# Kernel tuning notes

Hardware: AMD Instinct MI355X
Metric: run time of the kernel (lower is better)

Reference implementation:

```python
import jax, jax.numpy as jnp
import numpy as np

D_MODEL = 1024
NUM_HEADS = 16
THETA = 10000.0


def _rope(x, cos, sin):
    # x: [B, H, S, dk]; cos/sin: [B, 1, S, dk//2]
    x1 = x[..., 0::2]
    x2 = x[..., 1::2]
    r1 = x1 * cos - x2 * sin
    r2 = x1 * sin + x2 * cos
    return jnp.stack([r1, r2], axis=-1).reshape(x.shape)


def setup_inputs() -> dict:
    key = jax.random.key(0)
    ks = jax.random.split(key, 5)
    B, S, D = 2, 2048, D_MODEL
    std = np.sqrt(2.0 / (D + D))
    x = jax.random.normal(ks[0], (B, S, D), dtype=jnp.float32)
    Wq = jax.random.normal(ks[1], (D, D), dtype=jnp.float32) * std
    Wk = jax.random.normal(ks[2], (D, D), dtype=jnp.float32) * std
    Wv = jax.random.normal(ks[3], (D, D), dtype=jnp.float32) * std
    Wo = jax.random.normal(ks[4], (D, D), dtype=jnp.float32) * std
    token_positions = jnp.broadcast_to(jnp.arange(S, dtype=jnp.int32), (B, S))
    return {"x": x, "Wq": Wq, "Wk": Wk, "Wv": Wv, "Wo": Wo,
            "token_positions": token_positions}


def reference(x, Wq, Wk, Wv, Wo, token_positions):
    B, S, D = x.shape
    H = NUM_HEADS
    dk = D // H

    def split_heads(t):  # [B,S,D] -> [B,H,S,dk]
        return t.reshape(B, S, H, dk).transpose(0, 2, 1, 3)

    Q = split_heads(x @ Wq)
    K = split_heads(x @ Wk)
    V = split_heads(x @ Wv)

    # RoPE angles: theta^(-2i/dk) frequencies, indexed by token positions
    freqs = THETA ** (-jnp.arange(0, dk, 2, dtype=jnp.float32) / dk)  # [dk/2]
    angles = token_positions.astype(jnp.float32)[..., None] * freqs   # [B,S,dk/2]
    cos = jnp.cos(angles)[:, None]  # [B,1,S,dk/2] broadcast over heads
    sin = jnp.sin(angles)[:, None]
    Q = _rope(Q, cos, sin)
    K = _rope(K, cos, sin)

    scores = jnp.einsum('bhqd,bhkd->bhqk', Q, K) / jnp.sqrt(jnp.float32(dk))
    causal = jnp.tril(jnp.ones((S, S), dtype=bool))  # [S,S]
    scores = jnp.where(causal[None, None], scores, -jnp.inf)
    probs = jax.nn.softmax(scores, axis=-1)
    att = jnp.einsum('bhqk,bhkd->bhqd', probs, V)  # [B,H,S,dk]
    att = att.transpose(0, 2, 1, 3).reshape(B, S, D)
    return att @ Wo
```

## Files before the change

kernel.cpp:

```cpp
#include <hip/hip_runtime.h>
#include <math.h>

#define SLEN 2048
#define DMODEL 1024
#define NHEADS 16
#define DK 64
#define NBATCH 2
#define M_TOT (NBATCH * SLEN)
#define NQKV (3 * DMODEL)

typedef __bf16 bf16x8 __attribute__((ext_vector_type(8)));
typedef float f32x4 __attribute__((ext_vector_type(4)));
typedef float f32x16 __attribute__((ext_vector_type(16)));

static __device__ __forceinline__ unsigned short f2bf(float f) {
    unsigned int u = __float_as_uint(f);
    u += 0x7fffu + ((u >> 16) & 1u);
    return (unsigned short)(u >> 16);
}

static __device__ __forceinline__ unsigned cvtpk(float a, float b) {
    unsigned r;
    asm("v_cvt_pk_bf16_f32 %0, %1, %2" : "=v"(r) : "v"(a), "v"(b));
    return r;
}

#if __has_builtin(__builtin_amdgcn_exp2f)
#define EXP2(x) __builtin_amdgcn_exp2f(x)
#else
#define EXP2(x) exp2f(x)
#endif

static __device__ __forceinline__ void gload16(const void* g, void* l) {
    __builtin_amdgcn_global_load_lds(
        (const __attribute__((address_space(1))) unsigned int*)g,
        (__attribute__((address_space(3))) unsigned int*)l, 16, 0, 0);
}

__global__ __launch_bounds__(256)
void prep_all(const float* __restrict__ x,
              const float* __restrict__ Wq, const float* __restrict__ Wk,
              const float* __restrict__ Wv, const float* __restrict__ Wo,
              unsigned short* __restrict__ xb,
              unsigned short* __restrict__ Wcat,
              unsigned short* __restrict__ Wot)
{
    __shared__ float t[64][65];
    const int blk = blockIdx.x;
    const int tid = threadIdx.x;
    if (blk < 4096) {
        int i = blk * 256 + tid;
        float4 v = *(const float4*)&x[(size_t)i * 4];
        ushort4 o;
        o.x = f2bf(v.x); o.y = f2bf(v.y); o.z = f2bf(v.z); o.w = f2bf(v.w);
        *(ushort4*)&xb[(size_t)i * 4] = o;
    } else {
        const int tt = blk - 4096;
        const int widx = tt >> 8;
        const int t256 = tt & 255;
        const float* W = (widx == 0) ? Wq : (widx == 1) ? Wk : (widx == 2) ? Wv : Wo;
        unsigned short* Wt = (widx < 3) ? (Wcat + (size_t)widx * 1048576) : Wot;
        const int c0 = (t256 & 15) * 64, r0 = (t256 >> 4) * 64;
        const int tr = tid >> 4, tc = (tid & 15) * 4;
        #pragma unroll
        for (int rr = 0; rr < 4; ++rr) {
            int row = rr * 16 + tr;
            float4 v = *(const float4*)&W[(size_t)(r0 + row) * DMODEL + c0 + tc];
            t[row][tc + 0] = v.x; t[row][tc + 1] = v.y;
            t[row][tc + 2] = v.z; t[row][tc + 3] = v.w;
        }
        __syncthreads();
        #pragma unroll
        for (int rr = 0; rr < 4; ++rr) {
            int orow = rr * 16 + tr;
            ushort4 o;
            o.x = f2bf(t[tc + 0][orow]);
            o.y = f2bf(t[tc + 1][orow]);
            o.z = f2bf(t[tc + 2][orow]);
            o.w = f2bf(t[tc + 3][orow]);
            *(ushort4*)&Wt[(size_t)(c0 + orow) * DMODEL + r0 + tc] = o;
        }
    }
}

template<int BM, int BN, int MODE>
__global__ __launch_bounds__(256)
void gemm_mfma(const unsigned short* __restrict__ A,
               const unsigned short* __restrict__ Bt,
               float* __restrict__ C,
               unsigned short* __restrict__ Qd,
               unsigned short* __restrict__ Kd,
               unsigned short* __restrict__ Vtd,
               const int* __restrict__ pos,
               int N, int K)
{
    constexpr int MR = BM / 32;
    constexpr int NR = BN / 32;
    __shared__ unsigned short AB[(BM + BN) * 64];
    const int tid = threadIdx.x;
    const int w = tid >> 6, l = tid & 63;
    const int m0 = blockIdx.y * BM, n0 = blockIdx.x * BN;
    const int wr = (w >> 1) * (BM / 2), wc = (w & 1) * (BN / 2);
    const int lr = l >> 3, lp = l & 7;

    f32x4 acc[MR][NR] = {};

    unsigned short* As = AB;
    unsigned short* Bs = AB + BM * 64;

    for (int k0 = 0; k0 < K; k0 += 64) {
        #pragma unroll
        for (int i = 0; i < BM / 32; ++i) {
            int row = i * 32 + w * 8 + lr;
            int s = lp ^ (row & 7);
            gload16(A + (size_t)(m0 + row) * K + k0 + s * 8, (void*)(As + (i * 32 + w * 8) * 64));
        }
        #pragma unroll
        for (int i = 0; i < BN / 32; ++i) {
            int row = i * 32 + w * 8 + lr;
            int s = lp ^ (row & 7);
            gload16(Bt + (size_t)(n0 + row) * K + k0 + s * 8, (void*)(Bs + (i * 32 + w * 8) * 64));
        }
        __syncthreads();
        #pragma unroll
        for (int ks = 0; ks < 2; ++ks) {
            bf16x8 af[MR], bfr[NR];
            #pragma unroll
            for (int i = 0; i < MR; ++i) {
                int row = wr + i * 16 + (l & 15);
                int slot = (ks * 4 + (l >> 4)) ^ (row & 7);
                af[i] = *(const bf16x8*)((const char*)As + row * 128 + slot * 16);
            }
            #pragma unroll
            for (int j = 0; j < NR; ++j) {
                int row = wc + j * 16 + (l & 15);
                int slot = (ks * 4 + (l >> 4)) ^ (row & 7);
                bfr[j] = *(const bf16x8*)((const char*)Bs + row * 128 + slot * 16);
            }
            __builtin_amdgcn_s_setprio(1);
            #pragma unroll
            for (int i = 0; i < MR; ++i)
                #pragma unroll
                for (int j = 0; j < NR; ++j)
                    acc[i][j] = __builtin_amdgcn_mfma_f32_16x16x32_bf16(af[i], bfr[j], acc[i][j], 0, 0, 0);
            __builtin_amdgcn_s_setprio(0);
        }
        __syncthreads();
    }

    if (MODE == 0) {
        #pragma unroll
        for (int i = 0; i < MR; ++i)
            #pragma unroll
            for (int j = 0; j < NR; ++j)
                #pragma unroll
                for (int r = 0; r < 4; ++r) {
                    int row = m0 + wr + i * 16 + (l >> 4) * 4 + r;
                    int col = n0 + wc + j * 16 + (l & 15);
                    C[(size_t)row * N + col] = acc[i][j][r];
                }
    } else {
        const int seg = (n0 + wc) >> 10;
        #pragma unroll
        for (int i = 0; i < MR; ++i) {
            const int mbase = m0 + wr + i * 16 + (l >> 4) * 4;
            #pragma unroll
            for (int j = 0; j < NR; ++j) {
                const int n = n0 + wc + j * 16 + (l & 15);
                const int h = (n >> 6) & 15;
                const int d = n & 63;
                if (seg < 2) {
                    unsigned short* dst = (seg == 0) ? Qd : Kd;
                    const int de = d & ~1;
                    const float freq = __expf((float)de * (-9.210340371976184f / 64.f));
                    #pragma unroll
                    for (int r = 0; r < 4; ++r) {
                        const int m = mbase + r;
                        const int b = m >> 11, s = m & 2047;
                        float v = acc[i][j][r];
                        float p2 = __shfl_xor(v, 1);
                        float ang = (float)pos[m] * freq;
                        float sn, cs;
                        __sincosf(ang, &sn, &cs);
                        float res = ((l & 1) == 0) ? (v * cs - p2 * sn) : (p2 * sn + v * cs);
                        if (seg == 0) res *= 0.18033688011112042f;
                        dst[((size_t)(b * NHEADS + h) * SLEN + s) * DK + d] = f2bf(res);
                    }
                } else {
                    const int b = mbase >> 11, s0 = mbase & 2047;
                    const int tile = s0 >> 5, ksv = (s0 >> 4) & 1, hb = (s0 >> 3) & 1, j0 = s0 & 7;
                    const int mt2v = d >> 5, c31v = d & 31;
                    size_t idx = (size_t)(b * NHEADS + h) * 131072 + tile * 2048
                               + ksv * 1024 + mt2v * 512 + hb * 256 + c31v * 8 + j0;
                    ushort4 o;
                    o.x = f2bf(acc[i][j][0]); o.y = f2bf(acc[i][j][1]);
                    o.z = f2bf(acc[i][j][2]); o.w = f2bf(acc[i][j][3]);
                    *(ushort4*)&Vtd[idx] = o;
                }
            }
        }
    }
}

__global__ __launch_bounds__(128)
void attn_mfma(const unsigned short* __restrict__ Q,
               const unsigned short* __restrict__ K,
               const unsigned short* __restrict__ Vf,
               unsigned short* __restrict__ Oa)
{
    __shared__ char smem[17408];
    const int tid = threadIdx.x;
    const int w = tid >> 6, l = tid & 63;
    const int h = l >> 5, c31 = l & 31;

    const int id = blockIdx.x;
    const int bh = (id & 7) * 4 + ((id >> 3) & 3);
    const int g  = 63 - (id >> 5);
    const int n_w = (g >= w) ? ((g - w) >> 1) + 1 : 0;

    const unsigned short* Qb  = Q  + (size_t)bh * SLEN * DK;
    const unsigned short* Kb  = K  + (size_t)bh * SLEN * DK;
    const unsigned short* VfB = Vf + (size_t)bh * 131072;

    const int q_g = g * 32 + c31;

    bf16x8 qf[4];
    #pragma unroll
    for (int kb = 0; kb < 4; ++kb)
        qf[kb] = *(const bf16x8*)(Qb + (size_t)q_g * DK + kb * 16 + h * 8);

    float lsum = 0.f;
    f32x16 oacc[2] = {};

    char* mybuf = smem + w * 8192;
    auto STAGE = [&](int t, int p) {
        char* dst = mybuf + p * 4096;
        const unsigned short* src = Kb + (size_t)t * 2048;
        #pragma unroll
        for (int i2 = 0; i2 < 4; ++i2) {
            int row = i2 * 8 + (l >> 3);
            gload16(src + row * 64 + (((l & 7) ^ (row & 7)) * 8), dst + i2 * 1024);
        }
    };

    if (n_w > 0) {
        STAGE(w, 0);
        if (n_w > 1) STAGE(w + 2, 1);

        for (int i = 0; i < n_w; ++i) {
            const int t = w + 2 * i;
            const bool last = (i == n_w - 1);
            if (last) { asm volatile("s_waitcnt vmcnt(0)" ::: "memory"); }
            else      { asm volatile("s_waitcnt vmcnt(4)" ::: "memory"); }
            __builtin_amdgcn_sched_barrier(0);

            bf16x8 vf0, vf1, vf2, vf3;
            {
                const unsigned short* vsrc = VfB + (size_t)t * 2048 + l * 8;
                vf0 = *(const bf16x8*)(vsrc);
                vf1 = *(const bf16x8*)(vsrc + 512);
                vf2 = *(const bf16x8*)(vsrc + 1024);
                vf3 = *(const bf16x8*)(vsrc + 1536);
            }

            const char* kbuf = mybuf + (i & 1) * 4096;
            f32x16 sacc = {};
            __builtin_amdgcn_s_setprio(1);
            #pragma unroll
            for (int kb = 0; kb < 4; ++kb) {
                bf16x8 kf = *(const bf16x8*)(kbuf + c31 * 128 + ((((kb * 2 + h)) ^ (c31 & 7)) << 4));
                sacc = __builtin_amdgcn_mfma_f32_32x32x16_bf16(kf, qf[kb], sacc, 0, 0, 0);
            }
            __builtin_amdgcn_s_setprio(0);

            if (last && w == (g & 1)) {
                #pragma unroll
                for (int r = 0; r < 16; ++r) {
                    int crow = (r & 3) + 8 * (r >> 2) + 4 * h;
                    if (crow > c31) sacc[r] = -1e30f;
                }
            }

            float ps = 0.f;
            #pragma unroll
            for (int r = 0; r < 16; ++r) {
                float e = EXP2(sacc[r]);
                sacc[r] = e;
                ps += e;
            }
            lsum += ps;

            #pragma unroll
            for (int ks = 0; ks < 2; ++ks) {
                const int rb = ks * 8;
                unsigned pk0 = cvtpk(sacc[rb + 0], sacc[rb + 1]);
                unsigned pk1 = cvtpk(sacc[rb + 2], sacc[rb + 3]);
                unsigned pk2 = cvtpk(sacc[rb + 4], sacc[rb + 5]);
                unsigned pk3 = cvtpk(sacc[rb + 6], sacc[rb + 7]);
                asm("v_permlane32_swap_b32 %0, %1" : "+v"(pk0), "+v"(pk2));
                asm("v_permlane32_swap_b32 %0, %1" : "+v"(pk1), "+v"(pk3));
                union { unsigned u[4]; bf16x8 v; } pf;
                pf.u[0] = pk0;
                pf.u[1] = pk1;
                pf.u[2] = pk2;
                pf.u[3] = pk3;
                __builtin_amdgcn_s_setprio(1);
                oacc[0] = __builtin_amdgcn_mfma_f32_32x32x16_bf16(ks ? vf2 : vf0, pf.v, oacc[0], 0, 0, 0);
                oacc[1] = __builtin_amdgcn_mfma_f32_32x32x16_bf16(ks ? vf3 : vf1, pf.v, oacc[1], 0, 0, 0);
                __builtin_amdgcn_s_setprio(0);
            }

            if (i + 2 < n_w) STAGE(w + 2 * (i + 2), i & 1);
        }
    }

    __syncthreads();
    float* Ll = (float*)(smem + 16384);
    Ll[(w * 2 + h) * 32 + c31] = lsum;
    __syncthreads();
    const float lstar = Ll[c31] + Ll[32 + c31] + Ll[64 + c31] + Ll[96 + c31];

    float* Op = (float*)smem;
    if (w == 0) {
        #pragma unroll
        for (int mt = 0; mt < 2; ++mt)
            #pragma unroll
            for (int r = 0; r < 16; ++r)
                Op[(mt * 16 + r) * 64 + l] = oacc[mt][r];
    }
    __syncthreads();
    if (w == 1) {
        const float inv = 1.f / lstar;
        unsigned short* Os = (unsigned short*)(smem + 8192);
        #pragma unroll
        for (int mt = 0; mt < 2; ++mt)
            #pragma unroll
            for (int rq = 0; rq < 4; ++rq) {
                float a0 = (Op[(mt * 16 + rq * 4 + 0) * 64 + l] + oacc[mt][rq * 4 + 0]) * inv;
                float a1 = (Op[(mt * 16 + rq * 4 + 1) * 64 + l] + oacc[mt][rq * 4 + 1]) * inv;
                float a2 = (Op[(mt * 16 + rq * 4 + 2) * 64 + l] + oacc[mt][rq * 4 + 2]) * inv;
                float a3 = (Op[(mt * 16 + rq * 4 + 3) * 64 + l] + oacc[mt][rq * 4 + 3]) * inv;
                uint2 pv;
                pv.x = cvtpk(a0, a1);
                pv.y = cvtpk(a2, a3);
                int dbyte = mt * 64 + rq * 16 + h * 8;
                *(uint2*)((char*)Os + c31 * 128 + (dbyte ^ ((c31 & 7) << 4))) = pv;
            }
        const int b = bh >> 4, hh = bh & 15;
        const int cc = l & 7;
        #pragma unroll
        for (int pp = 0; pp < 4; ++pp) {
            int row = pp * 8 + (l >> 3);
            uint4 vv = *(const uint4*)((const char*)Os + row * 128 + ((cc ^ (row & 7)) << 4));
            int srow = g * 32 + row;
            *(uint4*)&Oa[((size_t)(b * SLEN + srow)) * DMODEL + hh * DK + cc * 8] = vv;
        }
    }
}

extern "C" void kernel_launch(void* const* d_in, const int* in_sizes, int n_in,
                              void* d_out, int out_size, void* d_ws, size_t ws_size,
                              hipStream_t stream)
{
    const float* x  = (const float*)d_in[0];
    const float* Wq = (const float*)d_in[1];
    const float* Wk = (const float*)d_in[2];
    const float* Wv = (const float*)d_in[3];
    const float* Wo = (const float*)d_in[4];
    const int*  pos = (const int*)d_in[5];
    float* out = (float*)d_out;

    char* ws = (char*)d_ws;
    const size_t MB = 1024 * 1024;
    unsigned short* xb   = (unsigned short*)(ws);
    unsigned short* Wcat = (unsigned short*)(ws + 8 * MB);
    unsigned short* Wot  = (unsigned short*)(ws + 14 * MB);
    unsigned short* Qws  = (unsigned short*)(ws + 16 * MB);
    unsigned short* Kws  = (unsigned short*)(ws + 24 * MB);
    unsigned short* Vfws = (unsigned short*)(ws + 32 * MB);
    unsigned short* attb = (unsigned short*)(ws + 40 * MB);

    prep_all<<<5120, 256, 0, stream>>>(x, Wq, Wk, Wv, Wo, xb, Wcat, Wot);

    gemm_mfma<128, 128, 1><<<dim3(NQKV / 128, M_TOT / 128), 256, 0, stream>>>(
        xb, Wcat, nullptr, Qws, Kws, Vfws, pos, NQKV, DMODEL);

    attn_mfma<<<2048, 128, 0, stream>>>(Qws, Kws, Vfws, attb);

    gemm_mfma<64, 128, 0><<<dim3(DMODEL / 128, M_TOT / 64), 256, 0, stream>>>(
        attb, Wot, out, nullptr, nullptr, nullptr, nullptr, DMODEL, DMODEL);
}
```

Measured before the change: 100.00 us.

## Pre-pack weights in MFMA fragment order and load B directly to registers

The weight transpose/convert prep kernel now writes bf16 weights in a layout that matches the 16x16x32 MFMA B-operand fragment order. The GEMM then loads B fragments straight from global memory into registers, with no LDS staging, and its shared buffer holds only A. This removes LDS traffic and bank pressure for B and halves the GEMM's shared-memory footprint. In exchange, each wave now fetches B from global or L2 with no reuse across the waves of a block, and it adds register pressure.

Result: slower. 104.3 us (+4.3%).

```diff
diff --git a/kernel.cpp b/kernel.cpp
--- a/kernel.cpp
+++ b/kernel.cpp
@@ -70,15 +70,20 @@
             t[row][tc + 2] = v.z; t[row][tc + 3] = v.w;
         }
         __syncthreads();
+        const int t2 = (r0 >> 5) + (tc >> 5);
+        const int q  = (tc >> 3) & 3;
+        const int e  = tc & 7;
         #pragma unroll
         for (int rr = 0; rr < 4; ++rr) {
             int orow = rr * 16 + tr;
+            const int n = c0 + orow;
+            const int G = n >> 4, n15 = n & 15;
             ushort4 o;
             o.x = f2bf(t[tc + 0][orow]);
             o.y = f2bf(t[tc + 1][orow]);
             o.z = f2bf(t[tc + 2][orow]);
             o.w = f2bf(t[tc + 3][orow]);
-            *(ushort4*)&Wt[(size_t)(c0 + orow) * DMODEL + r0 + tc] = o;
+            *(ushort4*)&Wt[(size_t)G * 16384 + t2 * 512 + q * 128 + n15 * 8 + e] = o;
         }
     }
 }
@@ -86,7 +91,7 @@
 template<int BM, int BN, int MODE>
 __global__ __launch_bounds__(256)
 void gemm_mfma(const unsigned short* __restrict__ A,
-               const unsigned short* __restrict__ Bt,
+               const unsigned short* __restrict__ Wf,
                float* __restrict__ C,
                unsigned short* __restrict__ Qd,
                unsigned short* __restrict__ Kd,
@@ -96,7 +101,7 @@
 {
     constexpr int MR = BM / 32;
     constexpr int NR = BN / 32;
-    __shared__ unsigned short AB[(BM + BN) * 64];
+    __shared__ unsigned short As[BM * 64];
     const int tid = threadIdx.x;
     const int w = tid >> 6, l = tid & 63;
     const int m0 = blockIdx.y * BM, n0 = blockIdx.x * BN;
@@ -105,44 +110,40 @@
 
     f32x4 acc[MR][NR] = {};
 
-    unsigned short* As = AB;
-    unsigned short* Bs = AB + BM * 64;
+    const unsigned short* wfB0 = Wf + ((size_t)((n0 + wc) >> 4)) * 16384 + l * 8;
 
     for (int k0 = 0; k0 < K; k0 += 64) {
+        bf16x8 bfr[NR][2];
+        {
+            const unsigned short* wfB = wfB0 + (k0 >> 5) * 512;
+            #pragma unroll
+            for (int j = 0; j < NR; ++j)
+                #pragma unroll
+                for (int ks = 0; ks < 2; ++ks)
+                    bfr[j][ks] = *(const bf16x8*)(wfB + j * 16384 + ks * 512);
+        }
         #pragma unroll
         for (int i = 0; i < BM / 32; ++i) {
             int row = i * 32 + w * 8 + lr;
             int s = lp ^ (row & 7);
             gload16(A + (size_t)(m0 + row) * K + k0 + s * 8, (void*)(As + (i * 32 + w * 8) * 64));
         }
-        #pragma unroll
-        for (int i = 0; i < BN / 32; ++i) {
-            int row = i * 32 + w * 8 + lr;
-            int s = lp ^ (row & 7);
-            gload16(Bt + (size_t)(n0 + row) * K + k0 + s * 8, (void*)(Bs + (i * 32 + w * 8) * 64));
-        }
         __syncthreads();
         #pragma unroll
         for (int ks = 0; ks < 2; ++ks) {
-            bf16x8 af[MR], bfr[NR];
+            bf16x8 af[MR];
             #pragma unroll
             for (int i = 0; i < MR; ++i) {
                 int row = wr + i * 16 + (l & 15);
                 int slot = (ks * 4 + (l >> 4)) ^ (row & 7);
                 af[i] = *(const bf16x8*)((const char*)As + row * 128 + slot * 16);
             }
-            #pragma unroll
-            for (int j = 0; j < NR; ++j) {
-                int row = wc + j * 16 + (l & 15);
-                int slot = (ks * 4 + (l >> 4)) ^ (row & 7);
-                bfr[j] = *(const bf16x8*)((const char*)Bs + row * 128 + slot * 16);
-            }
             __builtin_amdgcn_s_setprio(1);
             #pragma unroll
             for (int i = 0; i < MR; ++i)
                 #pragma unroll
                 for (int j = 0; j < NR; ++j)
-                    acc[i][j] = __builtin_amdgcn_mfma_f32_16x16x32_bf16(af[i], bfr[j], acc[i][j], 0, 0, 0);
+                    acc[i][j] = __builtin_amdgcn_mfma_f32_16x16x32_bf16(af[i], bfr[j][ks], acc[i][j], 0, 0, 0);
             __builtin_amdgcn_s_setprio(0);
         }
         __syncthreads();
```

## Pre-swizzle QKV weights into MFMA fragment layout and load B directly to registers

Applied to the files above, without the earlier changes.

The prep kernel now writes the Q/K/V weights in a fragment-ordered layout, so each lane's bf16x8 MFMA operand is contiguous. The QKV GEMM reads these B fragments straight from global memory into registers instead of staging them in LDS, and stages only A in shared memory with a K-step of 128. The aim is to cut LDS traffic and barrier pressure for the B operand and to halve the number of K iterations. In exchange, register use rises (16 B fragments per thread), which may lower occupancy and expose global load latency because B loads are not prefetched ahead of use.

Result: slower. 111.0 us (+11.0%).

```diff
diff --git a/kernel.cpp b/kernel.cpp
--- a/kernel.cpp
+++ b/kernel.cpp
@@ -59,7 +59,6 @@
         const int widx = tt >> 8;
         const int t256 = tt & 255;
         const float* W = (widx == 0) ? Wq : (widx == 1) ? Wk : (widx == 2) ? Wv : Wo;
-        unsigned short* Wt = (widx < 3) ? (Wcat + (size_t)widx * 1048576) : Wot;
         const int c0 = (t256 & 15) * 64, r0 = (t256 >> 4) * 64;
         const int tr = tid >> 4, tc = (tid & 15) * 4;
         #pragma unroll
@@ -70,32 +69,144 @@
             t[row][tc + 2] = v.z; t[row][tc + 3] = v.w;
         }
         __syncthreads();
-        #pragma unroll
-        for (int rr = 0; rr < 4; ++rr) {
-            int orow = rr * 16 + tr;
-            ushort4 o;
-            o.x = f2bf(t[tc + 0][orow]);
-            o.y = f2bf(t[tc + 1][orow]);
-            o.z = f2bf(t[tc + 2][orow]);
-            o.w = f2bf(t[tc + 3][orow]);
-            *(ushort4*)&Wt[(size_t)(c0 + orow) * DMODEL + r0 + tc] = o;
-        }
-    }
-}
-
-template<int BM, int BN, int MODE>
+        if (widx < 3) {
+            unsigned short* Wt = Wcat + (size_t)widx * 1048576;
+            const int t2 = (r0 >> 5) + (tc >> 5);
+            const int q  = (tc >> 3) & 3;
+            const int e  = tc & 7;
+            #pragma unroll
+            for (int rr = 0; rr < 4; ++rr) {
+                int orow = rr * 16 + tr;
+                const int n = c0 + orow;
+                const int G = n >> 4, n15 = n & 15;
+                ushort4 o;
+                o.x = f2bf(t[tc + 0][orow]);
+                o.y = f2bf(t[tc + 1][orow]);
+                o.z = f2bf(t[tc + 2][orow]);
+                o.w = f2bf(t[tc + 3][orow]);
+                *(ushort4*)&Wt[(size_t)G * 16384 + t2 * 512 + q * 128 + n15 * 8 + e] = o;
+            }
+        } else {
+            #pragma unroll
+            for (int rr = 0; rr < 4; ++rr) {
+                int orow = rr * 16 + tr;
+                ushort4 o;
+                o.x = f2bf(t[tc + 0][orow]);
+                o.y = f2bf(t[tc + 1][orow]);
+                o.z = f2bf(t[tc + 2][orow]);
+                o.w = f2bf(t[tc + 3][orow]);
+                *(ushort4*)&Wot[(size_t)(c0 + orow) * DMODEL + r0 + tc] = o;
+            }
+        }
+    }
+}
+
 __global__ __launch_bounds__(256)
-void gemm_mfma(const unsigned short* __restrict__ A,
-               const unsigned short* __restrict__ Bt,
-               float* __restrict__ C,
-               unsigned short* __restrict__ Qd,
-               unsigned short* __restrict__ Kd,
-               unsigned short* __restrict__ Vtd,
-               const int* __restrict__ pos,
-               int N, int K)
+void gemm_qkv(const unsigned short* __restrict__ A,
+              const unsigned short* __restrict__ Wf,
+              unsigned short* __restrict__ Qd,
+              unsigned short* __restrict__ Kd,
+              unsigned short* __restrict__ Vtd,
+              const int* __restrict__ pos)
 {
-    constexpr int MR = BM / 32;
-    constexpr int NR = BN / 32;
+    __shared__ unsigned short As[128 * 128];
+    const int tid = threadIdx.x;
+    const int w = tid >> 6, l = tid & 63;
+    const int m0 = blockIdx.y * 128, n0 = blockIdx.x * 128;
+    const int wr = (w >> 1) * 64, wc = (w & 1) * 64;
+
+    f32x4 acc[4][4] = {};
+
+    const unsigned short* wfB0 = Wf + ((size_t)((n0 + wc) >> 4)) * 16384 + l * 8;
+
+    const int srow = l >> 4;
+    const int sslot = l & 15;
+
+    for (int k0 = 0; k0 < 1024; k0 += 128) {
+        bf16x8 bfr[4][4];
+        {
+            const unsigned short* wfB = wfB0 + (k0 >> 5) * 512;
+            #pragma unroll
+            for (int j = 0; j < 4; ++j)
+                #pragma unroll
+                for (int ks = 0; ks < 4; ++ks)
+                    bfr[j][ks] = *(const bf16x8*)(wfB + j * 16384 + ks * 512);
+        }
+        #pragma unroll
+        for (int i = 0; i < 8; ++i) {
+            int row = w * 32 + i * 4 + srow;
+            gload16(A + (size_t)(m0 + row) * 1024 + k0 + ((sslot ^ (row & 7)) << 3),
+                    (void*)(As + (w * 32 + i * 4) * 128));
+        }
+        __syncthreads();
+        #pragma unroll
+        for (int ks = 0; ks < 4; ++ks) {
+            bf16x8 af[4];
+            #pragma unroll
+            for (int i = 0; i < 4; ++i) {
+                int row = wr + i * 16 + (l & 15);
+                int slot = (ks * 4 + (l >> 4)) ^ (row & 7);
+                af[i] = *(const bf16x8*)((const char*)As + row * 256 + slot * 16);
+            }
+            __builtin_amdgcn_s_setprio(1);
+            #pragma unroll
+            for (int i = 0; i < 4; ++i)
+                #pragma unroll
+                for (int j = 0; j < 4; ++j)
+                    acc[i][j] = __builtin_amdgcn_mfma_f32_16x16x32_bf16(af[i], bfr[j][ks], acc[i][j], 0, 0, 0);
+            __builtin_amdgcn_s_setprio(0);
+        }
+        __syncthreads();
+    }
+
+    const int seg = (n0 + wc) >> 10;
+    #pragma unroll
+    for (int i = 0; i < 4; ++i) {
+        const int mbase = m0 + wr + i * 16 + (l >> 4) * 4;
+        #pragma unroll
+        for (int j = 0; j < 4; ++j) {
+            const int n = n0 + wc + j * 16 + (l & 15);
+            const int h = (n >> 6) & 15;
+            const int d = n & 63;
+            if (seg < 2) {
+                unsigned short* dst = (seg == 0) ? Qd : Kd;
+                const int de = d & ~1;
+                const float freq = __expf((float)de * (-9.210340371976184f / 64.f));
+                #pragma unroll
+                for (int r = 0; r < 4; ++r) {
+                    const int m = mbase + r;
+                    const int b = m >> 11, s = m & 2047;
+                    float v = acc[i][j][r];
+                    float p2 = __shfl_xor(v, 1);
+                    float ang = (float)pos[m] * freq;
+                    float sn, cs;
+                    __sincosf(ang, &sn, &cs);
+                    float res = ((l & 1) == 0) ? (v * cs - p2 * sn) : (p2 * sn + v * cs);
+                    if (seg == 0) res *= 0.18033688011112042f;
+                    dst[((size_t)(b * NHEADS + h) * SLEN + s) * DK + d] = f2bf(res);
+                }
+            } else {
+                const int b = mbase >> 11, s0 = mbase & 2047;
+                const int tile = s0 >> 5, ksv = (s0 >> 4) & 1, hb = (s0 >> 3) & 1, j0 = s0 & 7;
+                const int mt2v = d >> 5, c31v = d & 31;
+                size_t idx = (size_t)(b * NHEADS + h) * 131072 + tile * 2048
+                           + ksv * 1024 + mt2v * 512 + hb * 256 + c31v * 8 + j0;
+                ushort4 o;
+                o.x = f2bf(acc[i][j][0]); o.y = f2bf(acc[i][j][1]);
+                o.z = f2bf(acc[i][j][2]); o.w = f2bf(acc[i][j][3]);
+                *(ushort4*)&Vtd[idx] = o;
+            }
+        }
+    }
+}
+
+__global__ __launch_bounds__(256)
+void gemm_wo(const unsigned short* __restrict__ A,
+             const unsigned short* __restrict__ Bt,
+             float* __restrict__ C, int N, int K)
+{
+    constexpr int BM = 64, BN = 128;
+    constexpr int MR = BM / 32, NR = BN / 32;
     __shared__ unsigned short AB[(BM + BN) * 64];
     const int tid = threadIdx.x;
     const int w = tid >> 6, l = tid & 63;
@@ -148,58 +259,16 @@
         __syncthreads();
     }
 
-    if (MODE == 0) {
-        #pragma unroll
-        for (int i = 0; i < MR; ++i)
-            #pragma unroll
-            for (int j = 0; j < NR; ++j)
-                #pragma unroll
-                for (int r = 0; r < 4; ++r) {
-                    int row = m0 + wr + i * 16 + (l >> 4) * 4 + r;
-                    int col = n0 + wc + j * 16 + (l & 15);
-                    C[(size_t)row * N + col] = acc[i][j][r];
-                }
-    } else {
-        const int seg = (n0 + wc) >> 10;
-        #pragma unroll
-        for (int i = 0; i < MR; ++i) {
-            const int mbase = m0 + wr + i * 16 + (l >> 4) * 4;
-            #pragma unroll
-            for (int j = 0; j < NR; ++j) {
-                const int n = n0 + wc + j * 16 + (l & 15);
-                const int h = (n >> 6) & 15;
-                const int d = n & 63;
-                if (seg < 2) {
-                    unsigned short* dst = (seg == 0) ? Qd : Kd;
-                    const int de = d & ~1;
-                    const float freq = __expf((float)de * (-9.210340371976184f / 64.f));
-                    #pragma unroll
-                    for (int r = 0; r < 4; ++r) {
-                        const int m = mbase + r;
-                        const int b = m >> 11, s = m & 2047;
-                        float v = acc[i][j][r];
-                        float p2 = __shfl_xor(v, 1);
-                        float ang = (float)pos[m] * freq;
-                        float sn, cs;
-                        __sincosf(ang, &sn, &cs);
-                        float res = ((l & 1) == 0) ? (v * cs - p2 * sn) : (p2 * sn + v * cs);
-                        if (seg == 0) res *= 0.18033688011112042f;
-                        dst[((size_t)(b * NHEADS + h) * SLEN + s) * DK + d] = f2bf(res);
-                    }
-                } else {
-                    const int b = mbase >> 11, s0 = mbase & 2047;
-                    const int tile = s0 >> 5, ksv = (s0 >> 4) & 1, hb = (s0 >> 3) & 1, j0 = s0 & 7;
-                    const int mt2v = d >> 5, c31v = d & 31;
-                    size_t idx = (size_t)(b * NHEADS + h) * 131072 + tile * 2048
-                               + ksv * 1024 + mt2v * 512 + hb * 256 + c31v * 8 + j0;
-                    ushort4 o;
-                    o.x = f2bf(acc[i][j][0]); o.y = f2bf(acc[i][j][1]);
-                    o.z = f2bf(acc[i][j][2]); o.w = f2bf(acc[i][j][3]);
-                    *(ushort4*)&Vtd[idx] = o;
-                }
-            }
-        }
-    }
+    #pragma unroll
+    for (int i = 0; i < MR; ++i)
+        #pragma unroll
+        for (int j = 0; j < NR; ++j)
+            #pragma unroll
+            for (int r = 0; r < 4; ++r) {
+                int row = m0 + wr + i * 16 + (l >> 4) * 4 + r;
+                int col = n0 + wc + j * 16 + (l & 15);
+                C[(size_t)row * N + col] = acc[i][j][r];
+            }
 }
 
 __global__ __launch_bounds__(128)
@@ -382,11 +451,11 @@
 
     prep_all<<<5120, 256, 0, stream>>>(x, Wq, Wk, Wv, Wo, xb, Wcat, Wot);
 
-    gemm_mfma<128, 128, 1><<<dim3(NQKV / 128, M_TOT / 128), 256, 0, stream>>>(
-        xb, Wcat, nullptr, Qws, Kws, Vfws, pos, NQKV, DMODEL);
+    gemm_qkv<<<dim3(NQKV / 128, M_TOT / 128), 256, 0, stream>>>(
+        xb, Wcat, Qws, Kws, Vfws, pos);
 
     attn_mfma<<<2048, 128, 0, stream>>>(Qws, Kws, Vfws, attb);
 
-    gemm_mfma<64, 128, 0><<<dim3(DMODEL / 128, M_TOT / 64), 256, 0, stream>>>(
-        attb, Wot, out, nullptr, nullptr, nullptr, nullptr, DMODEL, DMODEL);
-}
+    gemm_wo<<<dim3(DMODEL / 128, M_TOT / 64), 256, 0, stream>>>(
+        attb, Wot, out, DMODEL, DMODEL);
+}
```
